# Kernel optimization log

Hardware: AMD Instinct MI355X
Metric: run time of the kernel (lower is better)

The kernel has to match this reference:

```python
import jax, jax.numpy as jnp
import numpy as np

B, S, CIN, COUT, W, M, P = 32, 8192, 2, 1, 64, 16, 24


def setup_inputs() -> dict:
    key = jax.random.key(0)
    ks = jax.random.split(key, 12)

    def lin(k, o, i):
        return (jax.random.uniform(k, (o, i), jnp.float32) * 2 - 1) / np.float32(np.sqrt(i))

    scale = np.float32(1.0 / (W * W))  # SpectralConv1d init scale 1/(in*out)
    return {
        "x": jax.random.normal(ks[0], (B, S, CIN), jnp.float32),
        "fc0_w": lin(ks[1], W, CIN),
        "fc0_b": jnp.zeros((W,), jnp.float32),
        "conv_wr": jax.random.uniform(ks[2], (4, W, W, M), jnp.float32) * scale,
        "conv_wi": jax.random.uniform(ks[3], (4, W, W, M), jnp.float32) * scale,
        "pw_w": lin(ks[4], 4 * W, W).reshape(4, W, W),  # 1x1 conv weights (out,in)
        "pw_b": jnp.zeros((4, W), jnp.float32),
        "fc1_w": lin(ks[5], 128, W),
        "fc1_b": jnp.zeros((128,), jnp.float32),
        "fc2_w": lin(ks[6], COUT, 128),
        "ica_w": lin(ks[7], P, 128),
        "ica_b": jnp.zeros((P,), jnp.float32),
    }


def spectral_conv(h, wr, wi, n):
    # h: (B, W, S). Keep first M rfft modes, complex-multiply, inverse rfft.
    xf = jnp.fft.rfft(h, axis=-1)[..., :M]          # (B, W, M) complex
    w = wr + 1j * wi                                 # (W, W, M)
    of = jnp.einsum('bix,iox->box', xf, w)           # (B, W, M)
    of = jnp.pad(of, ((0, 0), (0, 0), (0, n // 2 + 1 - M)))
    return jnp.fft.irfft(of, n=n, axis=-1)


def reference(x, fc0_w, fc0_b, conv_wr, conv_wi, pw_w, pw_b, fc1_w, fc1_b, fc2_w, ica_w, ica_b):
    b, s, _ = x.shape
    h = x @ fc0_w.T + fc0_b                          # lift: (B, S, W)
    h = h.transpose(0, 2, 1)                         # (B, W, S)
    for l in range(4):
        x1 = spectral_conv(h, conv_wr[l], conv_wi[l], s)
        x2 = jnp.einsum('oi,bis->bos', pw_w[l], h) + pw_b[l][None, :, None]
        h = x1 + x2
        if l < 3:                                    # no relu after layer 3 (as in torch code)
            h = jax.nn.relu(h)
    h = h.transpose(0, 2, 1)                         # (B, S, W)
    h = h @ fc1_w.T + fc1_b                          # (B, S, 128)
    h_ = jax.nn.relu(h)
    # broadcast ICA decomposition: (B,S,1,128)*(1,1,COUT,128)
    components = h_[:, :, None, :] * fc2_w[None, None, :, :]
    tc = components @ ica_w.T + ica_b                # (B, S, COUT, P)
    out = tc.sum(-1)                                 # (B, S, COUT)
    return out, tc
```

## Files before the change

kernel.cpp:

```cpp
#include <hip/hip_runtime.h>
#include <math.h>

#define SB 8192
#define NB 32
#define WC 64
#define NM 16
#define NKC 32
#define NP 24
#define LP 132


__global__ __launch_bounds__(256) void k_table(float* __restrict__ T) {
    int s = blockIdx.x * 256 + threadIdx.x;
    float* row = T + (size_t)s * NKC;
    #pragma unroll
    for (int k = 0; k < NM; ++k) {
        int m = (k * s) & (SB - 1);
        double ang = (double)m * (6.283185307179586476925286766559 / (double)SB);
        row[2 * k]     = (float)cos(ang);
        row[2 * k + 1] = (float)sin(ang);
    }
}

__global__ __launch_bounds__(256) void k_prep(const float* __restrict__ ica_w,
                                              const float* __restrict__ fc2_w,
                                              float* __restrict__ icaT) {
    int tid = blockIdx.x * 256 + threadIdx.x;
    int c = tid / NP;
    int p = tid - c * NP;
    icaT[c * NP + p] = ica_w[p * 128 + c] * fc2_w[c];
}

__global__ __launch_bounds__(256) void k_prepw(const float* __restrict__ pw_w,
                                               float* __restrict__ pwT) {
    int tid = blockIdx.x * 256 + threadIdx.x;
    int l = tid >> 12, k = (tid >> 6) & 63, o = tid & 63;
    pwT[tid] = pw_w[(size_t)l * 4096 + o * 64 + k];
}

__global__ __launch_bounds__(256) void k_lift(const float* __restrict__ x,
                                              const float* __restrict__ fc0_w,
                                              const float* __restrict__ fc0_b,
                                              float* __restrict__ h,
                                              const float* __restrict__ T,
                                              float* __restrict__ xfp) {
    __shared__ float u[12544];
    int t = threadIdx.x;
    int b = blockIdx.y;
    int s0 = blockIdx.x * 128;
    int sl = t & 127, half = t >> 7;
    int cb = half * 32;

    float2 xv = ((const float2*)x)[(size_t)b * SB + s0 + sl];
    float* hcol = h + (size_t)b * WC * SB + s0 + sl;
    #pragma unroll
    for (int c = 0; c < 32; ++c) {
        int ch = cb + c;
        float v = fmaf(xv.x, fc0_w[2 * ch], fmaf(xv.y, fc0_w[2 * ch + 1], fc0_b[ch]));
        hcol[(size_t)ch * SB] = v;
        u[sl * 65 + ch] = v;
    }
    {
        int sl2 = t >> 1, jj0 = (t & 1) * 16;
        const float4* src = (const float4*)(T + (size_t)(s0 + sl2) * NKC + jj0);
        float4 a = src[0], c4 = src[1], d = src[2], e = src[3];
        float* Tt = u + 8320;
        Tt[(jj0 +  0) * LP + sl2] = a.x;  Tt[(jj0 +  1) * LP + sl2] = a.y;
        Tt[(jj0 +  2) * LP + sl2] = a.z;  Tt[(jj0 +  3) * LP + sl2] = a.w;
        Tt[(jj0 +  4) * LP + sl2] = c4.x; Tt[(jj0 +  5) * LP + sl2] = c4.y;
        Tt[(jj0 +  6) * LP + sl2] = c4.z; Tt[(jj0 +  7) * LP + sl2] = c4.w;
        Tt[(jj0 +  8) * LP + sl2] = d.x;  Tt[(jj0 +  9) * LP + sl2] = d.y;
        Tt[(jj0 + 10) * LP + sl2] = d.z;  Tt[(jj0 + 11) * LP + sl2] = d.w;
        Tt[(jj0 + 12) * LP + sl2] = e.x;  Tt[(jj0 + 13) * LP + sl2] = e.y;
        Tt[(jj0 + 14) * LP + sl2] = e.z;  Tt[(jj0 + 15) * LP + sl2] = e.w;
    }
    __syncthreads();

    int lane = t & 63;
    int wv = __builtin_amdgcn_readfirstlane(t >> 6);
    int g  = lane >> 3;
    int j8 = lane & 7;

    float dacc[8][4];
    #pragma unroll
    for (int i = 0; i < 8; ++i)
        #pragma unroll
        for (int m = 0; m < 4; ++m) dacc[i][m] = 0.f;

    #pragma unroll 4
    for (int ss = 0; ss < 32; ++ss) {
        int s = wv * 32 + ss;
        float tv0 = u[8320 + (j8 * 4 + 0) * LP + s];
        float tv1 = u[8320 + (j8 * 4 + 1) * LP + s];
        float tv2 = u[8320 + (j8 * 4 + 2) * LP + s];
        float tv3 = u[8320 + (j8 * 4 + 3) * LP + s];
        float4 h0 = *(const float4*)&u[s * 65 + g * 8];
        float4 h1 = *(const float4*)&u[s * 65 + g * 8 + 4];
        float hh[8] = {h0.x, h0.y, h0.z, h0.w, h1.x, h1.y, h1.z, h1.w};
        #pragma unroll
        for (int i = 0; i < 8; ++i) {
            dacc[i][0] = fmaf(hh[i], tv0, dacc[i][0]);
            dacc[i][1] = fmaf(hh[i], tv1, dacc[i][1]);
            dacc[i][2] = fmaf(hh[i], tv2, dacc[i][2]);
            dacc[i][3] = fmaf(hh[i], tv3, dacc[i][3]);
        }
    }

    __syncthreads();
    {
        float* slot = u + (wv * 64 + lane) * 33;
        #pragma unroll
        for (int i = 0; i < 8; ++i)
            #pragma unroll
            for (int m = 0; m < 4; ++m) slot[i * 4 + m] = dacc[i][m];
    }
    __syncthreads();

    float* dst = xfp + ((size_t)(blockIdx.x * NB + b)) * 2048;
    float res[8];
    #pragma unroll
    for (int e = 0; e < 8; ++e) {
        int idx = t * 8 + e;
        int ch = idx >> 5, mode = idx & 31;
        int g2 = ch >> 3, i2 = ch & 7;
        int q2 = mode >> 2, m2 = mode & 3;
        int lane2 = g2 * 8 + q2;
        int v2 = i2 * 4 + m2;
        res[e] = u[lane2 * 33 + v2] + u[(64 + lane2) * 33 + v2]
               + u[(128 + lane2) * 33 + v2] + u[(192 + lane2) * 33 + v2];
    }
    float4* d4 = (float4*)(dst + t * 8);
    d4[0] = make_float4(res[0], res[1], res[2], res[3]);
    d4[1] = make_float4(res[4], res[5], res[6], res[7]);
}

__global__ __launch_bounds__(256) void k_red(const float* __restrict__ xfp,
                                             float* __restrict__ xf, int nsc) {
    int idx = blockIdx.x * 256 + threadIdx.x;
    int b = idx >> 11;
    int r = idx & 2047;
    float s = 0.f;
    #pragma unroll 8
    for (int sc = 0; sc < nsc; ++sc)
        s += xfp[((size_t)(sc * NB + b)) * 2048 + r];
    xf[idx] = s;
}

__global__ __launch_bounds__(256) void k_mix(const float* __restrict__ xf,
                                             const float* __restrict__ wr,
                                             const float* __restrict__ wi,
                                             float* __restrict__ ofT) {
    int tid = blockIdx.x * 256 + threadIdx.x;
    int k = tid & 15;
    int o = (tid >> 4) & 63;
    int b = tid >> 10;
    float orr = 0.f, oii = 0.f;
    const float2* xfb = (const float2*)(xf + (size_t)b * WC * NKC);
    #pragma unroll 4
    for (int i = 0; i < WC; ++i) {
        float2 cs = xfb[i * NM + k];
        float wrv = wr[(i * WC + o) * NM + k];
        float wiv = wi[(i * WC + o) * NM + k];
        orr = fmaf(cs.x, wrv, fmaf(cs.y, wiv, orr));
        oii = fmaf(cs.x, wiv, fmaf(-cs.y, wrv, oii));
    }
    float alpha = (k == 0 ? 1.f : 2.f) / (float)SB;
    ofT[((size_t)b * NKC + 2 * k) * 64 + o]     = alpha * orr;
    ofT[((size_t)b * NKC + 2 * k + 1) * 64 + o] = -alpha * oii;
}

__global__ __launch_bounds__(256) void k_update(float* __restrict__ h,
                                                const float* __restrict__ T,
                                                const float* __restrict__ ofT,
                                                const float* __restrict__ pwT,
                                                const float* __restrict__ pwb,
                                                int relu, float* __restrict__ xfp,
                                                int dodft) {
    __shared__ float u[8448];
    float (*hS)[LP] = (float(*)[LP])u;
    int t = threadIdx.x;
    int b = blockIdx.y;
    int s0 = blockIdx.x * 128;
    int lane_s = t & 63;
    int g4 = __builtin_amdgcn_readfirstlane((t >> 6) & 3);
    int ob = g4 * 16;

    {
        int ch = t >> 2, part = t & 3;
        const float* hrow = h + ((size_t)(b * WC + ch)) * SB + s0;
        #pragma unroll
        for (int r = 0; r < 8; ++r) {
            int so = (part + 4 * r) * 4;
            *(float4*)&hS[ch][so] = *(const float4*)(hrow + so);
        }
    }
    __syncthreads();

    float acc0[16], acc1[16];
    #pragma unroll
    for (int o = 0; o < 16; ++o) { acc0[o] = pwb[ob + o]; acc1[o] = pwb[ob + o]; }

    const float* wbase0 = pwT + ob;
    const float* wbase1 = ofT + ((size_t)b * NKC) * 64 + ob;

    for (int kc = 0; kc < 8; ++kc) {
        #pragma unroll
        for (int uu = 0; uu < 8; ++uu) {
            int k = kc * 8 + uu;
            float h0 = hS[k][lane_s];
            float h1 = hS[k][64 + lane_s];
            const float* w = wbase0 + k * 64;
            #pragma unroll
            for (int o = 0; o < 16; ++o) {
                acc0[o] = fmaf(w[o], h0, acc0[o]);
                acc1[o] = fmaf(w[o], h1, acc1[o]);
            }
        }
    }
    const float4* Trow0 = (const float4*)(T + (size_t)(s0 + lane_s) * NKC);
    const float4* Trow1 = (const float4*)(T + (size_t)(s0 + 64 + lane_s) * NKC);
    for (int kc = 0; kc < 4; ++kc) {
        float4 v0 = Trow0[kc * 2], v1 = Trow0[kc * 2 + 1];
        float4 w0 = Trow1[kc * 2], w1v = Trow1[kc * 2 + 1];
        float xs0[8] = {v0.x, v0.y, v0.z, v0.w, v1.x, v1.y, v1.z, v1.w};
        float xs1[8] = {w0.x, w0.y, w0.z, w0.w, w1v.x, w1v.y, w1v.z, w1v.w};
        #pragma unroll
        for (int uu = 0; uu < 8; ++uu) {
            int j = kc * 8 + uu;
            const float* w = wbase1 + j * 64;
            #pragma unroll
            for (int o = 0; o < 16; ++o) {
                acc0[o] = fmaf(w[o], xs0[uu], acc0[o]);
                acc1[o] = fmaf(w[o], xs1[uu], acc1[o]);
            }
        }
    }

    if (relu) {
        #pragma unroll
        for (int o = 0; o < 16; ++o) {
            acc0[o] = fmaxf(acc0[o], 0.f);
            acc1[o] = fmaxf(acc1[o], 0.f);
        }
    }

    float* hw0 = h + (size_t)b * WC * SB + s0 + lane_s;
    float* hw1 = hw0 + 64;
    #pragma unroll
    for (int o = 0; o < 16; ++o) {
        hw0[(size_t)(ob + o) * SB] = acc0[o];
        hw1[(size_t)(ob + o) * SB] = acc1[o];
    }

    if (!dodft) return;

    __syncthreads();
    #pragma unroll
    for (int o = 0; o < 16; ++o) {
        u[lane_s * 65 + ob + o]        = acc0[o];
        u[(64 + lane_s) * 65 + ob + o] = acc1[o];
    }
    __syncthreads();

    int lane = t & 63;
    int wv = __builtin_amdgcn_readfirstlane(t >> 6);
    int g  = lane >> 3;
    int j8 = lane & 7;

    float dacc[8][4];
    #pragma unroll
    for (int i = 0; i < 8; ++i)
        #pragma unroll
        for (int m = 0; m < 4; ++m) dacc[i][m] = 0.f;

    #pragma unroll 4
    for (int ss = 0; ss < 32; ++ss) {
        int s = wv * 32 + ss;
        float4 tv = *(const float4*)(T + (size_t)(s0 + s) * NKC + j8 * 4);
        float4 h0 = *(const float4*)&u[s * 65 + g * 8];
        float4 h1 = *(const float4*)&u[s * 65 + g * 8 + 4];
        float hh[8] = {h0.x, h0.y, h0.z, h0.w, h1.x, h1.y, h1.z, h1.w};
        #pragma unroll
        for (int i = 0; i < 8; ++i) {
            dacc[i][0] = fmaf(hh[i], tv.x, dacc[i][0]);
            dacc[i][1] = fmaf(hh[i], tv.y, dacc[i][1]);
            dacc[i][2] = fmaf(hh[i], tv.z, dacc[i][2]);
            dacc[i][3] = fmaf(hh[i], tv.w, dacc[i][3]);
        }
    }

    __syncthreads();
    {
        float* slot = u + (wv * 64 + lane) * 33;
        #pragma unroll
        for (int i = 0; i < 8; ++i)
            #pragma unroll
            for (int m = 0; m < 4; ++m) slot[i * 4 + m] = dacc[i][m];
    }
    __syncthreads();

    float* dst = xfp + ((size_t)(blockIdx.x * NB + b)) * 2048;
    float res[8];
    #pragma unroll
    for (int e = 0; e < 8; ++e) {
        int idx = t * 8 + e;
        int ch = idx >> 5, mode = idx & 31;
        int g2 = ch >> 3, i2 = ch & 7;
        int q2 = mode >> 2, m2 = mode & 3;
        int lane2 = g2 * 8 + q2;
        int v2 = i2 * 4 + m2;
        res[e] = u[lane2 * 33 + v2] + u[(64 + lane2) * 33 + v2]
               + u[(128 + lane2) * 33 + v2] + u[(192 + lane2) * 33 + v2];
    }
    float4* d4 = (float4*)(dst + t * 8);
    d4[0] = make_float4(res[0], res[1], res[2], res[3]);
    d4[1] = make_float4(res[4], res[5], res[6], res[7]);
}

__global__ __launch_bounds__(256) void k_final(const float* __restrict__ h,
                                               const float* __restrict__ fc1_w,
                                               const float* __restrict__ fc1_b,
                                               const float* __restrict__ icaT,
                                               const float* __restrict__ ica_b,
                                               float* __restrict__ out,
                                               float* __restrict__ tc) {
    __shared__ float u_lds[4352];
    float (*hS)[68] = (float(*)[68])u_lds;
    int t = threadIdx.x;
    int b = blockIdx.y;
    int s0 = blockIdx.x * 64;
    int lane_s = t & 63;
    int wv = __builtin_amdgcn_readfirstlane(t >> 6);
    int c0 = wv * 32;

    {
        int sl = t & 63, chg = t >> 6;
        const float* hb = h + (size_t)b * WC * SB + s0 + sl;
        #pragma unroll
        for (int cc = 0; cc < 16; ++cc) {
            int ch = chg * 16 + cc;
            hS[sl][ch] = hb[(size_t)ch * SB];
        }
    }
    __syncthreads();

    float acc[NP];
    #pragma unroll
    for (int p = 0; p < NP; ++p) acc[p] = 0.f;

    for (int cq = 0; cq < 8; ++cq) {
        int c = c0 + 4 * cq;
        float tv0 = fc1_b[c], tv1 = fc1_b[c + 1], tv2 = fc1_b[c + 2], tv3 = fc1_b[c + 3];
        const float* w0 = fc1_w + (size_t)c * WC;
        const float* w1 = w0 + WC;
        const float* w2 = w1 + WC;
        const float* w3 = w2 + WC;
        for (int ioct = 0; ioct < 8; ++ioct) {
            float4 xa = *(const float4*)&hS[lane_s][ioct * 8];
            float4 xb = *(const float4*)&hS[lane_s][ioct * 8 + 4];
            float xs[8] = {xa.x, xa.y, xa.z, xa.w, xb.x, xb.y, xb.z, xb.w};
            #pragma unroll
            for (int uu = 0; uu < 8; ++uu) {
                int i = ioct * 8 + uu;
                tv0 = fmaf(w0[i], xs[uu], tv0);
                tv1 = fmaf(w1[i], xs[uu], tv1);
                tv2 = fmaf(w2[i], xs[uu], tv2);
                tv3 = fmaf(w3[i], xs[uu], tv3);
            }
        }
        tv0 = fmaxf(tv0, 0.f); tv1 = fmaxf(tv1, 0.f);
        tv2 = fmaxf(tv2, 0.f); tv3 = fmaxf(tv3, 0.f);
        const float* e0 = icaT + (size_t)c * NP;
        const float* e1 = e0 + NP;
        const float* e2 = e1 + NP;
        const float* e3 = e2 + NP;
        #pragma unroll
        for (int p = 0; p < NP; ++p)
            acc[p] = fmaf(tv0, e0[p], fmaf(tv1, e1[p],
                     fmaf(tv2, e2[p], fmaf(tv3, e3[p], acc[p]))));
    }

    __syncthreads();
    if (wv >= 2) {
        float* slot = u_lds + ((wv - 2) * 64 + lane_s) * 25;
        #pragma unroll
        for (int p = 0; p < NP; ++p) slot[p] = acc[p];
    }
    __syncthreads();
    if (wv < 2) {
        const float* slot = u_lds + (wv * 64 + lane_s) * 25;
        #pragma unroll
        for (int p = 0; p < NP; ++p) acc[p] += slot[p];
    }
    __syncthreads();
    if (wv == 1) {
        float* slot = u_lds + (64 + lane_s) * 25;
        #pragma unroll
        for (int p = 0; p < NP; ++p) slot[p] = acc[p];
    }
    __syncthreads();
    if (wv == 0) {
        const float* slot = u_lds + (64 + lane_s) * 25;
        #pragma unroll
        for (int p = 0; p < NP; ++p) acc[p] += slot[p] + ica_b[p];

        float osum = 0.f;
        #pragma unroll
        for (int p = 0; p < NP; ++p) osum += acc[p];
        size_t idx = (size_t)b * SB + s0 + lane_s;
        out[idx] = osum;

        float4* t4 = (float4*)(tc + idx * NP);
        t4[0] = make_float4(acc[0],  acc[1],  acc[2],  acc[3]);
        t4[1] = make_float4(acc[4],  acc[5],  acc[6],  acc[7]);
        t4[2] = make_float4(acc[8],  acc[9],  acc[10], acc[11]);
        t4[3] = make_float4(acc[12], acc[13], acc[14], acc[15]);
        t4[4] = make_float4(acc[16], acc[17], acc[18], acc[19]);
        t4[5] = make_float4(acc[20], acc[21], acc[22], acc[23]);
    }
}

extern "C" void kernel_launch(void* const* d_in, const int* in_sizes, int n_in,
                              void* d_out, int out_size, void* d_ws, size_t ws_size,
                              hipStream_t stream) {
    const float* x     = (const float*)d_in[0];
    const float* fc0_w = (const float*)d_in[1];
    const float* fc0_b = (const float*)d_in[2];
    const float* cwr   = (const float*)d_in[3];
    const float* cwi   = (const float*)d_in[4];
    const float* pw_w  = (const float*)d_in[5];
    const float* pw_b  = (const float*)d_in[6];
    const float* fc1_w = (const float*)d_in[7];
    const float* fc1_b = (const float*)d_in[8];
    const float* fc2_w = (const float*)d_in[9];
    const float* ica_w = (const float*)d_in[10];
    const float* ica_b = (const float*)d_in[11];

    float* out = (float*)d_out;
    float* tc  = out + (size_t)NB * SB;

    float* ws   = (float*)d_ws;
    float* h    = ws;
    float* T    = ws + 16777216;
    float* xf   = ws + 17039360;
    float* ofT  = ws + 17104896;
    float* icaT = ws + 17170432;
    float* pwT  = ws + 17173504;
    float* xfp  = tc;

    k_table<<<32, 256, 0, stream>>>(T);
    k_prep<<<12, 256, 0, stream>>>(ica_w, fc2_w, icaT);
    k_prepw<<<64, 256, 0, stream>>>(pw_w, pwT);
    k_lift<<<dim3(64, 32), 256, 0, stream>>>(x, fc0_w, fc0_b, h, T, xfp);

    for (int l = 0; l < 4; ++l) {
        k_red<<<256, 256, 0, stream>>>(xfp, xf, 64);
        k_mix<<<128, 256, 0, stream>>>(xf, cwr + (size_t)l * WC * WC * NM,
                                       cwi + (size_t)l * WC * WC * NM, ofT);
        k_update<<<dim3(64, 32), 256, 0, stream>>>(h, T, ofT,
                                                   pwT + (size_t)l * 4096,
                                                   pw_b + (size_t)l * WC,
                                                   (l < 3) ? 1 : 0,
                                                   xfp, (l < 3) ? 1 : 0);
    }

    k_final<<<dim3(128, 32), 256, 0, stream>>>(h, fc1_w, fc1_b, icaT, ica_b, out, tc);
}
```

Measured before the change: 386.4 us.

## Fuse spectral reduce and mode-mix kernels; read DFT table directly in lift

Merges the partial-DFT reduction kernel and the complex mode-mixing kernel into one per-batch kernel that sums the 64 partials into shared memory and then does the channel mixing with vectorized weight loads. This removes one launch per layer and the intermediate xf round trip. The fused kernel runs only 32 blocks, so the reduction gets far less parallelism than the previous 256-block version. Separately, the lift kernel now reads the twiddle table straight from global memory instead of staging it transposed in LDS, which shrinks shared memory use at the cost of uncoalesced per-lane global loads.

```diff
diff --git a/kernel.cpp b/kernel.cpp
--- a/kernel.cpp
+++ b/kernel.cpp
@@ -44,7 +44,7 @@
                                               float* __restrict__ h,
                                               const float* __restrict__ T,
                                               float* __restrict__ xfp) {
-    __shared__ float u[12544];
+    __shared__ float u[8448];
     int t = threadIdx.x;
     int b = blockIdx.y;
     int s0 = blockIdx.x * 128;
@@ -60,20 +60,6 @@
         hcol[(size_t)ch * SB] = v;
         u[sl * 65 + ch] = v;
     }
-    {
-        int sl2 = t >> 1, jj0 = (t & 1) * 16;
-        const float4* src = (const float4*)(T + (size_t)(s0 + sl2) * NKC + jj0);
-        float4 a = src[0], c4 = src[1], d = src[2], e = src[3];
-        float* Tt = u + 8320;
-        Tt[(jj0 +  0) * LP + sl2] = a.x;  Tt[(jj0 +  1) * LP + sl2] = a.y;
-        Tt[(jj0 +  2) * LP + sl2] = a.z;  Tt[(jj0 +  3) * LP + sl2] = a.w;
-        Tt[(jj0 +  4) * LP + sl2] = c4.x; Tt[(jj0 +  5) * LP + sl2] = c4.y;
-        Tt[(jj0 +  6) * LP + sl2] = c4.z; Tt[(jj0 +  7) * LP + sl2] = c4.w;
-        Tt[(jj0 +  8) * LP + sl2] = d.x;  Tt[(jj0 +  9) * LP + sl2] = d.y;
-        Tt[(jj0 + 10) * LP + sl2] = d.z;  Tt[(jj0 + 11) * LP + sl2] = d.w;
-        Tt[(jj0 + 12) * LP + sl2] = e.x;  Tt[(jj0 + 13) * LP + sl2] = e.y;
-        Tt[(jj0 + 14) * LP + sl2] = e.z;  Tt[(jj0 + 15) * LP + sl2] = e.w;
-    }
     __syncthreads();
 
     int lane = t & 63;
@@ -90,19 +76,16 @@
     #pragma unroll 4
     for (int ss = 0; ss < 32; ++ss) {
         int s = wv * 32 + ss;
-        float tv0 = u[8320 + (j8 * 4 + 0) * LP + s];
-        float tv1 = u[8320 + (j8 * 4 + 1) * LP + s];
-        float tv2 = u[8320 + (j8 * 4 + 2) * LP + s];
-        float tv3 = u[8320 + (j8 * 4 + 3) * LP + s];
+        float4 tv = *(const float4*)(T + (size_t)(s0 + s) * NKC + j8 * 4);
         float4 h0 = *(const float4*)&u[s * 65 + g * 8];
         float4 h1 = *(const float4*)&u[s * 65 + g * 8 + 4];
         float hh[8] = {h0.x, h0.y, h0.z, h0.w, h1.x, h1.y, h1.z, h1.w};
         #pragma unroll
         for (int i = 0; i < 8; ++i) {
-            dacc[i][0] = fmaf(hh[i], tv0, dacc[i][0]);
-            dacc[i][1] = fmaf(hh[i], tv1, dacc[i][1]);
-            dacc[i][2] = fmaf(hh[i], tv2, dacc[i][2]);
-            dacc[i][3] = fmaf(hh[i], tv3, dacc[i][3]);
+            dacc[i][0] = fmaf(hh[i], tv.x, dacc[i][0]);
+            dacc[i][1] = fmaf(hh[i], tv.y, dacc[i][1]);
+            dacc[i][2] = fmaf(hh[i], tv.z, dacc[i][2]);
+            dacc[i][3] = fmaf(hh[i], tv.w, dacc[i][3]);
         }
     }
 
@@ -134,39 +117,55 @@
     d4[1] = make_float4(res[4], res[5], res[6], res[7]);
 }
 
-__global__ __launch_bounds__(256) void k_red(const float* __restrict__ xfp,
-                                             float* __restrict__ xf, int nsc) {
-    int idx = blockIdx.x * 256 + threadIdx.x;
-    int b = idx >> 11;
-    int r = idx & 2047;
-    float s = 0.f;
-    #pragma unroll 8
-    for (int sc = 0; sc < nsc; ++sc)
-        s += xfp[((size_t)(sc * NB + b)) * 2048 + r];
-    xf[idx] = s;
-}
-
-__global__ __launch_bounds__(256) void k_mix(const float* __restrict__ xf,
-                                             const float* __restrict__ wr,
-                                             const float* __restrict__ wi,
-                                             float* __restrict__ ofT) {
-    int tid = blockIdx.x * 256 + threadIdx.x;
-    int k = tid & 15;
-    int o = (tid >> 4) & 63;
-    int b = tid >> 10;
-    float orr = 0.f, oii = 0.f;
-    const float2* xfb = (const float2*)(xf + (size_t)b * WC * NKC);
-    #pragma unroll 4
-    for (int i = 0; i < WC; ++i) {
-        float2 cs = xfb[i * NM + k];
-        float wrv = wr[(i * WC + o) * NM + k];
-        float wiv = wi[(i * WC + o) * NM + k];
-        orr = fmaf(cs.x, wrv, fmaf(cs.y, wiv, orr));
-        oii = fmaf(cs.x, wiv, fmaf(-cs.y, wrv, oii));
-    }
-    float alpha = (k == 0 ? 1.f : 2.f) / (float)SB;
-    ofT[((size_t)b * NKC + 2 * k) * 64 + o]     = alpha * orr;
-    ofT[((size_t)b * NKC + 2 * k + 1) * 64 + o] = -alpha * oii;
+__global__ __launch_bounds__(256) void k_redmix(const float* __restrict__ xfp,
+                                                const float* __restrict__ wr,
+                                                const float* __restrict__ wi,
+                                                float* __restrict__ ofT) {
+    __shared__ float xs[2048];
+    int b = blockIdx.x;
+    int t = threadIdx.x;
+
+    {
+        float a[8];
+        #pragma unroll
+        for (int e = 0; e < 8; ++e) a[e] = 0.f;
+        for (int sc = 0; sc < 64; ++sc) {
+            const float4* src = (const float4*)(xfp + ((size_t)(sc * NB + b)) * 2048) + t * 2;
+            float4 v0 = src[0], v1 = src[1];
+            a[0] += v0.x; a[1] += v0.y; a[2] += v0.z; a[3] += v0.w;
+            a[4] += v1.x; a[5] += v1.y; a[6] += v1.z; a[7] += v1.w;
+        }
+        #pragma unroll
+        for (int e = 0; e < 8; ++e) xs[t * 8 + e] = a[e];
+    }
+    __syncthreads();
+
+    int e0 = t * 4;
+    float orr[4] = {0.f, 0.f, 0.f, 0.f};
+    float oii[4] = {0.f, 0.f, 0.f, 0.f};
+    for (int i = 0; i < 64; ++i) {
+        float4 wrv = ((const float4*)(wr + (size_t)i * 1024))[t];
+        float4 wiv = ((const float4*)(wi + (size_t)i * 1024))[t];
+        float wrs[4] = {wrv.x, wrv.y, wrv.z, wrv.w};
+        float wis[4] = {wiv.x, wiv.y, wiv.z, wiv.w};
+        #pragma unroll
+        for (int q = 0; q < 4; ++q) {
+            int k = (e0 + q) & 15;
+            float cr = xs[i * 32 + 2 * k];
+            float ci = xs[i * 32 + 2 * k + 1];
+            orr[q] = fmaf(cr, wrs[q], fmaf(ci, wis[q], orr[q]));
+            oii[q] = fmaf(cr, wis[q], fmaf(-ci, wrs[q], oii[q]));
+        }
+    }
+    float* dstb = ofT + (size_t)b * NKC * 64;
+    #pragma unroll
+    for (int q = 0; q < 4; ++q) {
+        int e = e0 + q;
+        int k = e & 15, o = e >> 4;
+        float alpha = (k == 0 ? 1.f : 2.f) / (float)SB;
+        dstb[(2 * k) * 64 + o]     = alpha * orr[q];
+        dstb[(2 * k + 1) * 64 + o] = -alpha * oii[q];
+    }
 }
 
 __global__ __launch_bounds__(256) void k_update(float* __restrict__ h,
@@ -358,14 +357,14 @@
         for (int ioct = 0; ioct < 8; ++ioct) {
             float4 xa = *(const float4*)&hS[lane_s][ioct * 8];
             float4 xb = *(const float4*)&hS[lane_s][ioct * 8 + 4];
-            float xs[8] = {xa.x, xa.y, xa.z, xa.w, xb.x, xb.y, xb.z, xb.w};
+            float xsv[8] = {xa.x, xa.y, xa.z, xa.w, xb.x, xb.y, xb.z, xb.w};
             #pragma unroll
             for (int uu = 0; uu < 8; ++uu) {
                 int i = ioct * 8 + uu;
-                tv0 = fmaf(w0[i], xs[uu], tv0);
-                tv1 = fmaf(w1[i], xs[uu], tv1);
-                tv2 = fmaf(w2[i], xs[uu], tv2);
-                tv3 = fmaf(w3[i], xs[uu], tv3);
+                tv0 = fmaf(w0[i], xsv[uu], tv0);
+                tv1 = fmaf(w1[i], xsv[uu], tv1);
+                tv2 = fmaf(w2[i], xsv[uu], tv2);
+                tv3 = fmaf(w3[i], xsv[uu], tv3);
             }
         }
         tv0 = fmaxf(tv0, 0.f); tv1 = fmaxf(tv1, 0.f);
@@ -442,7 +441,6 @@
     float* ws   = (float*)d_ws;
     float* h    = ws;
     float* T    = ws + 16777216;
-    float* xf   = ws + 17039360;
     float* ofT  = ws + 17104896;
     float* icaT = ws + 17170432;
     float* pwT  = ws + 17173504;
@@ -454,9 +452,8 @@
     k_lift<<<dim3(64, 32), 256, 0, stream>>>(x, fc0_w, fc0_b, h, T, xfp);
 
     for (int l = 0; l < 4; ++l) {
-        k_red<<<256, 256, 0, stream>>>(xfp, xf, 64);
-        k_mix<<<128, 256, 0, stream>>>(xf, cwr + (size_t)l * WC * WC * NM,
-                                       cwi + (size_t)l * WC * WC * NM, ofT);
+        k_redmix<<<32, 256, 0, stream>>>(xfp, cwr + (size_t)l * WC * WC * NM,
+                                         cwi + (size_t)l * WC * WC * NM, ofT);
         k_update<<<dim3(64, 32), 256, 0, stream>>>(h, T, ofT,
                                                    pwT + (size_t)l * 4096,
                                                    pw_b + (size_t)l * WC,
```

Measured after the change: 399.6 us. 1.03x slower.
